# Kernel optimization log

Hardware: AMD Instinct MI355X
Metric: run time of the kernel (lower is better)

## Reference

```python
import jax, jax.numpy as jnp
import numpy as np

IN = 4096      # in_channels (unpacked)
OUT = 11008    # out_channels
GROUP = 128    # quantization group size
W_BIT = 4
PACK = 32 // W_BIT  # 8 int4 values per int32
N_GROUPS = IN // GROUP
BATCH = 64


def setup_inputs() -> dict:
    key = jax.random.key(0)
    k1, k2, k3, k4 = jax.random.split(key, 4)
    x = jax.random.normal(k1, (BATCH, IN), dtype=jnp.float32)
    # bit-packed int4 weights: 8 nibbles per int32, packed along input dim
    qweight = jax.random.randint(k2, (IN // PACK, OUT), 0, jnp.iinfo(jnp.int32).max, dtype=jnp.int32)
    scales = jax.random.uniform(k3, (N_GROUPS, OUT), dtype=jnp.float32) * 0.01 + 1e-3
    # zero points near mid-range of int4
    zeros = 7.5 + jax.random.uniform(k4, (N_GROUPS, OUT), dtype=jnp.float32) - 0.5
    g_idx = (jnp.arange(IN) // GROUP).astype(jnp.int32)
    return {"x": x, "qweight": qweight, "scales": scales, "zeros": zeros, "g_idx": g_idx}


def unpack_int4(qweight):
    # [IN//8, OUT] int32 -> [IN, OUT] float32 in [0, 15]
    shifts = (jnp.arange(PACK, dtype=jnp.int32) * W_BIT)  # [8]
    nibbles = (qweight[:, None, :] >> shifts[None, :, None]) & 0xF  # [IN//8, 8, OUT]
    return nibbles.reshape(IN, OUT).astype(jnp.float32)


def reference(x, qweight, scales, zeros, g_idx):
    w_int = unpack_int4(qweight)                       # [IN, OUT]
    W = (w_int - zeros[g_idx]) * scales[g_idx]         # group-wise dequant, [IN, OUT]
    return x @ W                                       # [BATCH, OUT]
```

## Files before the change

### kernel.cpp

```cpp
#include <hip/hip_runtime.h>
#include <hip/hip_fp16.h>
#include <stdint.h>


#define IN 4096
#define OUT 11008
#define BATCH 64
#define SPLITK 4
#define KSPL 1024
#define BN 64
#define GRID_N 172

typedef __attribute__((ext_vector_type(8))) __bf16 bf16x8;
typedef __attribute__((ext_vector_type(4))) float f32x4;

static __device__ __forceinline__ ushort f2bf(float f) {
  uint32_t u = __float_as_uint(f);
  u += 0x7fff + ((u >> 16) & 1);
  return (ushort)(u >> 16);
}
static __device__ __forceinline__ float bf2f(ushort h) {
  return __uint_as_float(((uint32_t)h) << 16);
}

__global__ void cvt_frag_kernel(const float* __restrict__ x,
                                ushort* __restrict__ xbf,
                                float* __restrict__ xsum) {
  const int g = blockIdx.x >> 2;
  const int mq = blockIdx.x & 3;
  const int t = threadIdx.x;
  const int m = mq * 16 + (t >> 2);
  const int q = t & 3;
  const int ks = 4 * g + q;
  const int kb = 32 * ks;

  float v[32];
  ushort vb[32];
  float s = 0.f;
#pragma unroll
  for (int c4 = 0; c4 < 8; ++c4) {
    float4 f = *(const float4*)&x[m * IN + kb + 4 * c4];
    v[4 * c4 + 0] = f.x; v[4 * c4 + 1] = f.y; v[4 * c4 + 2] = f.z; v[4 * c4 + 3] = f.w;
  }
#pragma unroll
  for (int c = 0; c < 32; ++c) {
    vb[c] = f2bf(v[c]);
    s += bf2f(vb[c]);
  }
  const int i = m >> 4, mlane = m & 15;
#pragma unroll
  for (int qd = 0; qd < 4; ++qd) {
    ushort o[8];
    o[0] = vb[8 * qd + 0]; o[1] = vb[8 * qd + 4];
    o[2] = vb[8 * qd + 1]; o[3] = vb[8 * qd + 5];
    o[4] = vb[8 * qd + 2]; o[5] = vb[8 * qd + 6];
    o[6] = vb[8 * qd + 3]; o[7] = vb[8 * qd + 7];
    const int flat = (ks * 4 + i) * 64 + qd * 16 + mlane;
    *(uint4*)&xbf[flat * 8] = *(uint4*)o;
  }
  s += __shfl_xor(s, 1);
  s += __shfl_xor(s, 2);
  if (q == 0) xsum[g * 64 + m] = s;
}

__global__ __launch_bounds__(256, 3) void mpq_gemm(
    const ushort* __restrict__ xbf,
    const int* __restrict__ qweight,
    const float* __restrict__ scales,
    const float* __restrict__ zeros,
    const float* __restrict__ xsum,
    __half* __restrict__ P)
{
  __shared__ uint4 A_lds[2048];

  const int n0 = blockIdx.x * BN;
  const int sp = blockIdx.y;
  const int k0 = sp * KSPL;
  const int tid = threadIdx.x;
  const int lane = tid & 63;
  const int w = tid >> 6;
  const int wm = w >> 1, wn = w & 1;
  const int mlane = lane & 15, quad = lane >> 4;
  const int ncol = n0 + 32 * wn + mlane;

  f32x4 macc[2][2] = {};

  const uint4* gA = (const uint4*)xbf + (size_t)(k0 / 32) * 256;

  for (int h = 0; h < 4; ++h) {
    uint32_t q[8][2];
    const int qrow0 = k0 / 8 + h * 32;
#pragma unroll
    for (int ks = 0; ks < 8; ++ks)
#pragma unroll
      for (int j = 0; j < 2; ++j)
        q[ks][j] = (uint32_t)qweight[(size_t)(qrow0 + ks * 4 + quad) * OUT + ncol + 16 * j];

    __syncthreads();
    const uint4* src = gA + (size_t)h * 2048;
#pragma unroll
    for (int it = 0; it < 8; ++it)
      A_lds[tid + 256 * it] = src[tid + 256 * it];
    __syncthreads();

#pragma unroll
    for (int g2 = 0; g2 < 2; ++g2) {
      f32x4 gacc[2][2] = {};
#pragma unroll
      for (int ksl = 0; ksl < 4; ++ksl) {
        const int ks = g2 * 4 + ksl;
        bf16x8 af[2];
#pragma unroll
        for (int i2 = 0; i2 < 2; ++i2)
          af[i2] = *(const bf16x8*)&A_lds[(ks * 4 + 2 * wm + i2) * 64 + lane];
#pragma unroll
        for (int j = 0; j < 2; ++j) {
          uint32_t p[4];
          p[0] = ( q[ks][j]        & 0x000F000Fu) | 0x43004300u;
          p[1] = ((q[ks][j] >>  4) & 0x000F000Fu) | 0x43004300u;
          p[2] = ((q[ks][j] >>  8) & 0x000F000Fu) | 0x43004300u;
          p[3] = ((q[ks][j] >> 12) & 0x000F000Fu) | 0x43004300u;
          bf16x8 bfr = *(bf16x8*)p;
#pragma unroll
          for (int i2 = 0; i2 < 2; ++i2)
            gacc[i2][j] = __builtin_amdgcn_mfma_f32_16x16x32_bf16(af[i2], bfr, gacc[i2][j], 0, 0, 0);
        }
      }
      const int g = (k0 >> 7) + h * 2 + g2;
      float Sv[2][4];
#pragma unroll
      for (int i2 = 0; i2 < 2; ++i2)
#pragma unroll
        for (int r = 0; r < 4; ++r)
          Sv[i2][r] = xsum[g * 64 + 32 * wm + 16 * i2 + 4 * quad + r];
#pragma unroll
      for (int j = 0; j < 2; ++j) {
        const float s = scales[g * OUT + ncol + 16 * j];
        const float z = zeros[g * OUT + ncol + 16 * j];
        const float u = s * (128.0f + z);
#pragma unroll
        for (int i2 = 0; i2 < 2; ++i2)
#pragma unroll
          for (int r = 0; r < 4; ++r)
            macc[i2][j][r] = fmaf(s, gacc[i2][j][r], fmaf(-u, Sv[i2][r], macc[i2][j][r]));
      }
    }
  }

  __half* Pp = P + (size_t)sp * (BATCH * OUT);
#pragma unroll
  for (int i2 = 0; i2 < 2; ++i2)
#pragma unroll
    for (int r = 0; r < 4; ++r) {
      const int m = 32 * wm + 16 * i2 + 4 * quad + r;
#pragma unroll
      for (int j = 0; j < 2; ++j)
        Pp[(size_t)m * OUT + ncol + 16 * j] = __float2half(macc[i2][j][r]);
    }
}

__global__ void reduce_kernel(const __half* __restrict__ P, float* __restrict__ out) {
  const int t = blockIdx.x * blockDim.x + threadIdx.x;
  float4 a = {0.f, 0.f, 0.f, 0.f};
  const uint2* P2 = (const uint2*)P;
#pragma unroll
  for (int s = 0; s < SPLITK; ++s) {
    uint2 v = P2[t + (size_t)s * (BATCH * OUT / 4)];
    const __half2 lo = *(const __half2*)&v.x;
    const __half2 hi = *(const __half2*)&v.y;
    float2 flo = __half22float2(lo), fhi = __half22float2(hi);
    a.x += flo.x; a.y += flo.y; a.z += fhi.x; a.w += fhi.y;
  }
  ((float4*)out)[t] = a;
}

extern "C" void kernel_launch(void* const* d_in, const int* in_sizes, int n_in,
                              void* d_out, int out_size, void* d_ws, size_t ws_size,
                              hipStream_t stream) {
  const float* x = (const float*)d_in[0];
  const int* qweight = (const int*)d_in[1];
  const float* scales = (const float*)d_in[2];
  const float* zeros = (const float*)d_in[3];
  float* out = (float*)d_out;
  ushort* xbf = (ushort*)d_ws;
  float* xsum = (float*)((char*)d_ws + (1 << 19));
  __half* P = (__half*)((char*)d_ws + (1 << 20));

  cvt_frag_kernel<<<128, 64, 0, stream>>>(x, xbf, xsum);
  mpq_gemm<<<dim3(GRID_N, SPLITK), 256, 0, stream>>>(xbf, qweight, scales, zeros, xsum, P);
  reduce_kernel<<<BATCH * OUT / 4 / 256, 256, 0, stream>>>(P, out);
}
```

Measured before the change: 94.23 us.

## Drop LDS staging of activations, double split-K, raise occupancy bound

Removes the shared-memory staging of the bf16 activation fragments and their __syncthreads barriers; each wave now loads its A fragments straight from global memory (L2-resident). Split-K goes from 4 to 8, with each block covering 512 K across four fully unrolled quantization groups. Launch bounds are raised to 4 blocks per SM. This adds parallelism and removes barrier stalls, at the cost of redundant A reads across waves and twice the fp16 partial-sum traffic for the reduce kernel, which still uses SPLITK.

```diff
diff --git a/kernel.cpp b/kernel.cpp
--- a/kernel.cpp
+++ b/kernel.cpp
@@ -6,8 +6,8 @@
 #define IN 4096
 #define OUT 11008
 #define BATCH 64
-#define SPLITK 4
-#define KSPL 1024
+#define SPLITK 8
+#define KSPL 512
 #define BN 64
 #define GRID_N 172
 
@@ -63,7 +63,7 @@
   if (q == 0) xsum[g * 64 + m] = s;
 }
 
-__global__ __launch_bounds__(256, 3) void mpq_gemm(
+__global__ __launch_bounds__(256, 4) void mpq_gemm(
     const ushort* __restrict__ xbf,
     const int* __restrict__ qweight,
     const float* __restrict__ scales,
@@ -71,8 +71,6 @@
     const float* __restrict__ xsum,
     __half* __restrict__ P)
 {
-  __shared__ uint4 A_lds[2048];
-
   const int n0 = blockIdx.x * BN;
   const int sp = blockIdx.y;
   const int k0 = sp * KSPL;
@@ -85,65 +83,62 @@
 
   f32x4 macc[2][2] = {};
 
-  const uint4* gA = (const uint4*)xbf + (size_t)(k0 / 32) * 256;
+#pragma unroll
+  for (int gl = 0; gl < 4; ++gl) {
+    const int g = (k0 >> 7) + gl;
 
-  for (int h = 0; h < 4; ++h) {
-    uint32_t q[8][2];
-    const int qrow0 = k0 / 8 + h * 32;
+    uint32_t q[4][2];
+    const int qrow0 = k0 / 8 + 16 * gl;
 #pragma unroll
-    for (int ks = 0; ks < 8; ++ks)
+    for (int ksl = 0; ksl < 4; ++ksl)
 #pragma unroll
       for (int j = 0; j < 2; ++j)
-        q[ks][j] = (uint32_t)qweight[(size_t)(qrow0 + ks * 4 + quad) * OUT + ncol + 16 * j];
+        q[ksl][j] = (uint32_t)qweight[(size_t)(qrow0 + 4 * ksl + quad) * OUT + ncol + 16 * j];
 
-    __syncthreads();
-    const uint4* src = gA + (size_t)h * 2048;
+    bf16x8 af[4][2];
+    const int slab0 = (k0 >> 5) + 4 * gl;
 #pragma unroll
-    for (int it = 0; it < 8; ++it)
-      A_lds[tid + 256 * it] = src[tid + 256 * it];
-    __syncthreads();
+    for (int ksl = 0; ksl < 4; ++ksl)
+#pragma unroll
+      for (int i2 = 0; i2 < 2; ++i2)
+        af[ksl][i2] = *(const bf16x8*)&xbf[(((slab0 + ksl) * 4 + 2 * wm + i2) * 64 + lane) * 8];
+
+    float sj[2], zj[2], Sv[2][4];
+#pragma unroll
+    for (int j = 0; j < 2; ++j) {
+      sj[j] = scales[g * OUT + ncol + 16 * j];
+      zj[j] = zeros[g * OUT + ncol + 16 * j];
+    }
+#pragma unroll
+    for (int i2 = 0; i2 < 2; ++i2)
+#pragma unroll
+      for (int r = 0; r < 4; ++r)
+        Sv[i2][r] = xsum[g * 64 + 32 * wm + 16 * i2 + 4 * quad + r];
+
+    f32x4 gacc[2][2] = {};
+#pragma unroll
+    for (int ksl = 0; ksl < 4; ++ksl)
+#pragma unroll
+      for (int j = 0; j < 2; ++j) {
+        uint32_t p[4];
+        p[0] = ( q[ksl][j]        & 0x000F000Fu) | 0x43004300u;
+        p[1] = ((q[ksl][j] >>  4) & 0x000F000Fu) | 0x43004300u;
+        p[2] = ((q[ksl][j] >>  8) & 0x000F000Fu) | 0x43004300u;
+        p[3] = ((q[ksl][j] >> 12) & 0x000F000Fu) | 0x43004300u;
+        bf16x8 bfr = *(bf16x8*)p;
+#pragma unroll
+        for (int i2 = 0; i2 < 2; ++i2)
+          gacc[i2][j] = __builtin_amdgcn_mfma_f32_16x16x32_bf16(af[ksl][i2], bfr, gacc[i2][j], 0, 0, 0);
+      }
 
 #pragma unroll
-    for (int g2 = 0; g2 < 2; ++g2) {
-      f32x4 gacc[2][2] = {};
-#pragma unroll
-      for (int ksl = 0; ksl < 4; ++ksl) {
-        const int ks = g2 * 4 + ksl;
-        bf16x8 af[2];
-#pragma unroll
-        for (int i2 = 0; i2 < 2; ++i2)
-          af[i2] = *(const bf16x8*)&A_lds[(ks * 4 + 2 * wm + i2) * 64 + lane];
-#pragma unroll
-        for (int j = 0; j < 2; ++j) {
-          uint32_t p[4];
-          p[0] = ( q[ks][j]        & 0x000F000Fu) | 0x43004300u;
-          p[1] = ((q[ks][j] >>  4) & 0x000F000Fu) | 0x43004300u;
-          p[2] = ((q[ks][j] >>  8) & 0x000F000Fu) | 0x43004300u;
-          p[3] = ((q[ks][j] >> 12) & 0x000F000Fu) | 0x43004300u;
-          bf16x8 bfr = *(bf16x8*)p;
-#pragma unroll
-          for (int i2 = 0; i2 < 2; ++i2)
-            gacc[i2][j] = __builtin_amdgcn_mfma_f32_16x16x32_bf16(af[i2], bfr, gacc[i2][j], 0, 0, 0);
-        }
-      }
-      const int g = (k0 >> 7) + h * 2 + g2;
-      float Sv[2][4];
+    for (int j = 0; j < 2; ++j) {
+      const float u = sj[j] * (128.0f + zj[j]);
 #pragma unroll
       for (int i2 = 0; i2 < 2; ++i2)
 #pragma unroll
         for (int r = 0; r < 4; ++r)
-          Sv[i2][r] = xsum[g * 64 + 32 * wm + 16 * i2 + 4 * quad + r];
-#pragma unroll
-      for (int j = 0; j < 2; ++j) {
-        const float s = scales[g * OUT + ncol + 16 * j];
-        const float z = zeros[g * OUT + ncol + 16 * j];
-        const float u = s * (128.0f + z);
-#pragma unroll
-        for (int i2 = 0; i2 < 2; ++i2)
-#pragma unroll
-          for (int r = 0; r < 4; ++r)
-            macc[i2][j][r] = fmaf(s, gacc[i2][j][r], fmaf(-u, Sv[i2][r], macc[i2][j][r]));
-      }
+          macc[i2][j][r] = fmaf(sj[j], gacc[i2][j][r], fmaf(-u, Sv[i2][r], macc[i2][j][r]));
     }
   }
 
```

After: 95.21 us. No clear change (+1.0%).
